# Optimization experiments

Hardware: AMD Instinct MI355X
Metric: run time of the kernel (lower is better)

Reference implementation:

```python
import jax, jax.numpy as jnp
import numpy as np

B, C, FULLBIN, T = 4, 2, 1025, 1024
BINS = 1024            # n_fft // 2
BANDS = 4
D = BINS // BANDS      # 256
FF = 2048
FF2, FF4 = FF // 2, FF // 4
CROP = 1024
EPS = 1e-5


def layernorm(x, g, b):
    m = jnp.mean(x, axis=-1, keepdims=True)
    v = jnp.mean(jnp.square(x - m), axis=-1, keepdims=True)
    return (x - m) * jax.lax.rsqrt(v + EPS) * g + b


def dconv(x, w, pad):
    # depthwise Conv1d: x (B, Cc, L), w (Cc, 1, K)
    return jax.lax.conv_general_dilated(
        x, w, window_strides=(1,), padding=[(pad, pad)],
        feature_group_count=x.shape[1],
        dimension_numbers=('NCH', 'OIH', 'NCH'))


def pconv(x, w):
    # pointwise Conv1d: x (B, Ci, L), w (Co, Ci, 1)
    return jnp.einsum('bcl,oc->bol', x, w[:, :, 0])


def reference(src, in_w, ln1_g, ln1_b, glu_w, ln2_g, ln2_b,
              c1L_dw, c1L_pw, c1R_dw, c1R_pw, ln3_g, ln3_b,
              c1M_dw, c1M_pw, ln4_g, ln4_b,
              q_w, q_b, qc_w, qc_b, k_w, k_b, v_w, v_b, o_w, o_b, er,
              ln5_g, ln5_b, c2_w, c3_w, out_w):
    s = src[:, :, :BINS]                                 # (B,C,F,T)
    x = jnp.einsum('bcft,c->btf', s, in_w[0])            # in_project + squeeze -> (B,T,BINS)

    # GLU block
    h = layernorm(x, ln1_g, ln1_b)
    g = h @ glu_w.T                                       # (B,T,2*BINS)
    x = x + g[..., :BINS] * jax.nn.sigmoid(g[..., BINS:])

    # conv feed-forward (note: conv1L applied without transpose, as in original)
    h = layernorm(x, ln2_g, ln2_b)
    hL = jax.nn.relu(pconv(dconv(h, c1L_dw, 5), c1L_pw))                          # (B,FF2,BINS)
    hR = jax.nn.relu(pconv(dconv(jnp.swapaxes(h, 1, 2), c1R_dw, 3), c1R_pw))      # (B,FF4,T)
    hR = jnp.swapaxes(hR, 1, 2)                                                   # (B,T,FF4)
    hR = jnp.pad(hR, ((0, 0), (0, 0), (0, BINS - FF4)))
    h = layernorm(hL + hR, ln3_g, ln3_b)                                          # (B,FF2,BINS)
    h = pconv(dconv(jnp.swapaxes(h, 1, 2), c1M_dw, 3), c1M_pw)                    # (B,BINS,FF2)
    x = x + jnp.swapaxes(h, 1, 2)

    # multiband frame attention (q_conv reused for q,k,v as in original)
    h = layernorm(x, ln4_g, ln4_b)

    def qkv(W, bvec):
        y = h @ W.T + bvec
        y = dconv(jnp.swapaxes(y, 1, 2), qc_w, 3) + qc_b[None, :, None]
        return jnp.swapaxes(y, 1, 2).reshape(B, T, BANDS, D)

    q = qkv(q_w, q_b).transpose(0, 2, 1, 3)              # (B,BANDS,T,D)
    k = qkv(k_w, k_b).transpose(0, 2, 3, 1)              # (B,BANDS,D,T)
    v = qkv(v_w, v_b).transpose(0, 2, 1, 3)              # (B,BANDS,T,D)

    p = jnp.pad(q @ er, ((0, 0), (0, 0), (0, 0), (1, 0)))  # (B,BANDS,T,CROP+1)
    p = jnp.swapaxes(p, 2, 3)[:, :, 1:, :]                 # (B,BANDS,CROP,T)
    qk = (q @ k + p) / jnp.sqrt(jnp.float32(BINS))
    a = jax.nn.softmax(qk, axis=-1)
    o = (a @ v).transpose(0, 2, 1, 3).reshape(B, T, BINS) @ o_w.T + o_b
    x = x + o

    # squared-ReLU MLP
    h = layernorm(x, ln5_g, ln5_b)
    h = jnp.square(jax.nn.relu(h @ c2_w.T)) @ c3_w.T
    x = x + h

    # stack back as extra channel, output head, ReLU1, replicate-pad freq row
    t = jnp.swapaxes(x, 1, 2)[:, None]                   # (B,1,BINS,T)
    s2 = jnp.concatenate([s, t], axis=1)                 # (B,C+1,BINS,T)
    y = jnp.einsum('bcft,oc->boft', s2, out_w)           # (B,2,BINS,T)
    y = jnp.clip(y, 0.0, 6.0) / 6.0
    return jnp.concatenate([y, y[:, :, -1:, :]], axis=2)  # (B,2,FULLBIN,T)


def setup_inputs() -> dict:
    key = jax.random.key(0)
    ks = jax.random.split(key, 20)
    n = lambda i, shape, s=0.02: jax.random.normal(ks[i], shape, jnp.float32) * s
    return {
        'src': jax.random.normal(ks[0], (B, C, FULLBIN, T), jnp.float32),
        'in_w': n(1, (1, C)),
        'ln1_g': jnp.ones((BINS,), jnp.float32), 'ln1_b': jnp.zeros((BINS,), jnp.float32),
        'glu_w': n(2, (2 * BINS, BINS)),
        'ln2_g': jnp.ones((BINS,), jnp.float32), 'ln2_b': jnp.zeros((BINS,), jnp.float32),
        'c1L_dw': n(3, (BINS, 1, 11), 0.1), 'c1L_pw': n(4, (FF2, BINS, 1)),
        'c1R_dw': n(5, (BINS, 1, 7), 0.1), 'c1R_pw': n(6, (FF4, BINS, 1)),
        'ln3_g': jnp.ones((FF2,), jnp.float32), 'ln3_b': jnp.zeros((FF2,), jnp.float32),
        'c1M_dw': n(7, (FF2, 1, 7), 0.1), 'c1M_pw': n(8, (BINS, FF2, 1)),
        'ln4_g': jnp.ones((BINS,), jnp.float32), 'ln4_b': jnp.zeros((BINS,), jnp.float32),
        'q_w': n(9, (BINS, BINS)), 'q_b': jnp.zeros((BINS,), jnp.float32),
        'qc_w': n(10, (BINS, 1, 7), 0.1), 'qc_b': jnp.zeros((BINS,), jnp.float32),
        'k_w': n(11, (BINS, BINS)), 'k_b': jnp.zeros((BINS,), jnp.float32),
        'v_w': n(12, (BINS, BINS)), 'v_b': jnp.zeros((BINS,), jnp.float32),
        'o_w': n(13, (BINS, BINS)), 'o_b': jnp.zeros((BINS,), jnp.float32),
        'er': jax.random.normal(ks[14], (D, CROP), jnp.float32),
        'ln5_g': jnp.ones((BINS,), jnp.float32), 'ln5_b': jnp.zeros((BINS,), jnp.float32),
        'c2_w': n(15, (FF, BINS)), 'c3_w': n(16, (BINS, FF)),
        'out_w': n(17, (2, C + 1)),
    }
```

## Files before the change

### kernel.cpp

```cpp
#include <hip/hip_runtime.h>
#include <math.h>


typedef unsigned short u16;
typedef __attribute__((ext_vector_type(4))) float floatx4;
typedef __attribute__((ext_vector_type(8))) short short8;

#define NB 4
static const long long M1 = 1024LL * 1024LL;

__device__ __forceinline__ float bf2f(u16 h) {
    union { unsigned int u; float f; } v;
    v.u = ((unsigned int)h) << 16;
    return v.f;
}
__device__ __forceinline__ u16 f2bf(float x) {
    union { float f; unsigned int u; } v;
    v.f = x;
    unsigned int r = (v.u + 0x7FFFu + ((v.u >> 16) & 1u)) >> 16;
    return (u16)r;
}

__device__ __forceinline__ void async_cp16(const u16* g, u16* lds) {
    __builtin_amdgcn_global_load_lds(
        (const __attribute__((address_space(1))) unsigned int*)g,
        (__attribute__((address_space(3))) unsigned int*)lds, 16, 0, 0);
}

__device__ __forceinline__ float block_sum(float v) {
    __shared__ float sd[4];
    #pragma unroll
    for (int off = 32; off; off >>= 1) v += __shfl_down(v, off, 64);
    int lane = threadIdx.x & 63, wid = threadIdx.x >> 6;
    __syncthreads();
    if (lane == 0) sd[wid] = v;
    __syncthreads();
    return sd[0] + sd[1] + sd[2] + sd[3];
}

template<int BM, int BN, int ACT, int OUT>
__global__ __launch_bounds__(256)
void gemm_bf(const u16* __restrict__ A, const u16* __restrict__ B,
             void* __restrict__ Cv, int K, int lda, int ldb, int ldc,
             long long sAz, long long sBz, long long sCz,
             const float* __restrict__ bias, float scale)
{
    constexpr int MI = BM / 32;
    constexpr int NJ = BN / 32;

    A += (long long)blockIdx.z * sAz;
    B += (long long)blockIdx.z * sBz;
    const long long zc = (long long)blockIdx.z * sCz;

    __shared__ u16 As[BM * 64];
    __shared__ u16 Bs[BN * 64];

    const int id = blockIdx.x + gridDim.x * blockIdx.y;
    const int bx = (id >> 3) % gridDim.x;
    const int by = (id & 7) + 8 * ((id >> 3) / gridDim.x);
    const int m0 = by * BM;
    const int n0 = bx * BN;

    const int lane = threadIdx.x & 63;
    const int w    = threadIdx.x >> 6;
    const int wm   = (w >> 1) * (BM / 2);
    const int wn   = (w & 1) * (BN / 2);
    const int srow = lane >> 2;
    const int scol = (lane & 3) * 8;

    floatx4 acc[MI][NJ];
    #pragma unroll
    for (int i = 0; i < MI; i++)
        #pragma unroll
        for (int j = 0; j < NJ; j++)
            acc[i][j] = floatx4{0.f, 0.f, 0.f, 0.f};

    for (int k0 = 0; k0 < K; k0 += 64) {
        #pragma unroll
        for (int r = 0; r < BM / 32; r++) {
            const int inst = w * (BM / 32) + r;
            const int rg = inst >> 1, kb = inst & 1;
            async_cp16(A + (long long)(m0 + rg * 16 + srow) * lda + k0 + kb * 32 + scol,
                       &As[(rg * 2 + kb) * 512]);
        }
        #pragma unroll
        for (int r = 0; r < BN / 32; r++) {
            const int inst = w * (BN / 32) + r;
            const int rg = inst >> 1, kb = inst & 1;
            async_cp16(B + (long long)(n0 + rg * 16 + srow) * ldb + k0 + kb * 32 + scol,
                       &Bs[(rg * 2 + kb) * 512]);
        }
        __syncthreads();

        #pragma unroll
        for (int s = 0; s < 2; s++) {
            short8 a[MI], b[NJ];
            const int fr = lane & 15;
            const int q  = lane >> 4;
            const int go = (fr * 4 + q) * 8;
            #pragma unroll
            for (int i = 0; i < MI; i++)
                a[i] = *(const short8*)&As[(((wm >> 4) + i) * 2 + s) * 512 + go];
            #pragma unroll
            for (int j = 0; j < NJ; j++)
                b[j] = *(const short8*)&Bs[(((wn >> 4) + j) * 2 + s) * 512 + go];
            #pragma unroll
            for (int i = 0; i < MI; i++)
                #pragma unroll
                for (int j = 0; j < NJ; j++)
                    acc[i][j] = __builtin_amdgcn_mfma_f32_16x16x32_bf16(
                        a[i], b[j], acc[i][j], 0, 0, 0);
        }
        __syncthreads();
    }

    float* Cf = (float*)Cv;
    u16*  Cb  = (u16*)Cv;
    const int cn    = n0 + wn + (lane & 15);
    const int rbase = m0 + wm + (lane >> 4) * 4;
    float bj[NJ];
    #pragma unroll
    for (int j = 0; j < NJ; j++) bj[j] = bias ? bias[cn + j * 16] : 0.f;

    #pragma unroll
    for (int i = 0; i < MI; i++) {
        #pragma unroll
        for (int r = 0; r < 4; r++) {
            const int m = rbase + i * 16 + r;
            #pragma unroll
            for (int j = 0; j < NJ; j++) {
                const int n = cn + j * 16;
                float v = (acc[i][j][r] + bj[j]) * scale;
                if (ACT == 1) v = fmaxf(v, 0.f);
                else if (ACT == 2) { v = fmaxf(v, 0.f); v = v * v; }
                const long long ci = zc + (long long)m * ldc + n;
                if (OUT == 0)      Cf[ci] = v;
                else if (OUT == 1) Cf[ci] += v;
                else if (OUT == 2) Cb[ci] = f2bf(v);
                else               Cb[ci] = f2bf(bf2f(Cb[ci]) + v);
            }
        }
    }
}

__global__ __launch_bounds__(256)
void glugemm_k(const u16* __restrict__ A, const u16* __restrict__ B1,
               const u16* __restrict__ B2, u16* __restrict__ X)
{
    constexpr int BM = 128, BN = 64, MI = 4, NJ = 2;
    __shared__ u16 As[BM * 64];
    __shared__ u16 B1s[BN * 64];
    __shared__ u16 B2s[BN * 64];

    const int id = blockIdx.x + gridDim.x * blockIdx.y;
    const int bx = (id >> 3) % gridDim.x;
    const int by = (id & 7) + 8 * ((id >> 3) / gridDim.x);
    const int m0 = by * BM;
    const int n0 = bx * BN;

    const int lane = threadIdx.x & 63;
    const int w    = threadIdx.x >> 6;
    const int wm   = (w >> 1) * 64;
    const int wn   = (w & 1) * 32;
    const int srow = lane >> 2;
    const int scol = (lane & 3) * 8;

    floatx4 acc1[MI][NJ], acc2[MI][NJ];
    #pragma unroll
    for (int i = 0; i < MI; i++)
        #pragma unroll
        for (int j = 0; j < NJ; j++) {
            acc1[i][j] = floatx4{0.f, 0.f, 0.f, 0.f};
            acc2[i][j] = floatx4{0.f, 0.f, 0.f, 0.f};
        }

    for (int k0 = 0; k0 < 1024; k0 += 64) {
        #pragma unroll
        for (int r = 0; r < 4; r++) {
            const int inst = w * 4 + r;
            const int rg = inst >> 1, kb = inst & 1;
            async_cp16(A + (long long)(m0 + rg * 16 + srow) * 1024 + k0 + kb * 32 + scol,
                       &As[(rg * 2 + kb) * 512]);
        }
        #pragma unroll
        for (int r = 0; r < 2; r++) {
            const int inst = w * 2 + r;
            const int rg = inst >> 1, kb = inst & 1;
            async_cp16(B1 + (long long)(n0 + rg * 16 + srow) * 1024 + k0 + kb * 32 + scol,
                       &B1s[(rg * 2 + kb) * 512]);
            async_cp16(B2 + (long long)(n0 + rg * 16 + srow) * 1024 + k0 + kb * 32 + scol,
                       &B2s[(rg * 2 + kb) * 512]);
        }
        __syncthreads();

        #pragma unroll
        for (int s = 0; s < 2; s++) {
            short8 a[MI], b1[NJ], b2[NJ];
            const int fr = lane & 15;
            const int q  = lane >> 4;
            const int go = (fr * 4 + q) * 8;
            #pragma unroll
            for (int i = 0; i < MI; i++)
                a[i] = *(const short8*)&As[(((wm >> 4) + i) * 2 + s) * 512 + go];
            #pragma unroll
            for (int j = 0; j < NJ; j++) {
                b1[j] = *(const short8*)&B1s[(((wn >> 4) + j) * 2 + s) * 512 + go];
                b2[j] = *(const short8*)&B2s[(((wn >> 4) + j) * 2 + s) * 512 + go];
            }
            #pragma unroll
            for (int i = 0; i < MI; i++)
                #pragma unroll
                for (int j = 0; j < NJ; j++) {
                    acc1[i][j] = __builtin_amdgcn_mfma_f32_16x16x32_bf16(
                        a[i], b1[j], acc1[i][j], 0, 0, 0);
                    acc2[i][j] = __builtin_amdgcn_mfma_f32_16x16x32_bf16(
                        a[i], b2[j], acc2[i][j], 0, 0, 0);
                }
        }
        __syncthreads();
    }

    const int cn    = n0 + wn + (lane & 15);
    const int rbase = m0 + wm + (lane >> 4) * 4;
    #pragma unroll
    for (int i = 0; i < MI; i++)
        #pragma unroll
        for (int r = 0; r < 4; r++) {
            const int m = rbase + i * 16 + r;
            #pragma unroll
            for (int j = 0; j < NJ; j++) {
                const int n = cn + j * 16;
                float g = acc1[i][j][r] / (1.f + expf(-acc2[i][j][r]));
                u16* xp = &X[(long long)m * 1024 + n];
                *xp = f2bf(bf2f(*xp) + g);
            }
        }
}

__global__ __launch_bounds__(256)
void sgemm_exp_k(const u16* __restrict__ Qpk, const u16* __restrict__ Kpk,
                 const u16* __restrict__ ErT,
                 u16* __restrict__ S, float* __restrict__ rowsum, float scale)
{
    constexpr int MI = 4, NJ = 4;
    const int i0 = blockIdx.x;
    const int x  = i0 & 7;
    const int j0 = i0 >> 3;
    const int z  = x + 8 * (j0 & 1);
    const int t  = j0 >> 1;
    const int bx = t & 7, by = t >> 3;

    const u16* Aq = Qpk + (long long)z * 262144;
    const u16* Bk = Kpk + (long long)z * 262144;
    S += (long long)z * M1;
    rowsum += z << 10;

    __shared__ u16 As[128 * 64];
    __shared__ u16 Bs[128 * 64];

    const int m0 = by * 128;
    const int n0 = bx * 128;

    const int lane = threadIdx.x & 63;
    const int w    = threadIdx.x >> 6;
    const int wm   = (w >> 1) * 64;
    const int wn   = (w & 1) * 64;
    const int srow = lane >> 2;
    const int scol = (lane & 3) * 8;

    floatx4 acc[MI][NJ];
    #pragma unroll
    for (int i = 0; i < MI; i++)
        #pragma unroll
        for (int j = 0; j < NJ; j++)
            acc[i][j] = floatx4{0.f, 0.f, 0.f, 0.f};

    for (int k0 = 0; k0 < 512; k0 += 64) {
        #pragma unroll
        for (int r = 0; r < 4; r++) {
            const int inst = w * 4 + r;
            const int rg = inst >> 1, kb = inst & 1;
            const int cb = k0 + kb * 32;
            const int ra = m0 + rg * 16 + srow;
            const u16* sa = (cb < 256)
                ? Aq  + (long long)ra * 256 + cb + scol
                : ErT + (long long)ra * 256 + (cb - 256) + scol;
            async_cp16(sa, &As[(rg * 2 + kb) * 512]);
            const int rb = n0 + rg * 16 + srow;
            const u16* sb = (cb < 256)
                ? Bk + (long long)rb * 256 + cb + scol
                : Aq + (long long)rb * 256 + (cb - 256) + scol;
            async_cp16(sb, &Bs[(rg * 2 + kb) * 512]);
        }
        __syncthreads();
        #pragma unroll
        for (int s = 0; s < 2; s++) {
            short8 a[MI], b[NJ];
            const int fr = lane & 15;
            const int q  = lane >> 4;
            const int go = (fr * 4 + q) * 8;
            #pragma unroll
            for (int i = 0; i < MI; i++)
                a[i] = *(const short8*)&As[(((wm >> 4) + i) * 2 + s) * 512 + go];
            #pragma unroll
            for (int j = 0; j < NJ; j++)
                b[j] = *(const short8*)&Bs[(((wn >> 4) + j) * 2 + s) * 512 + go];
            #pragma unroll
            for (int i = 0; i < MI; i++)
                #pragma unroll
                for (int j = 0; j < NJ; j++)
                    acc[i][j] = __builtin_amdgcn_mfma_f32_16x16x32_bf16(
                        a[i], b[j], acc[i][j], 0, 0, 0);
        }
        __syncthreads();
    }

    const int cn    = n0 + wn + (lane & 15);
    const int rbase = m0 + wm + (lane >> 4) * 4;
    #pragma unroll
    for (int i = 0; i < MI; i++)
        #pragma unroll
        for (int r = 0; r < 4; r++) {
            const int m = rbase + i * 16 + r;
            float part = 0.f;
            #pragma unroll
            for (int j = 0; j < NJ; j++) {
                const int n = cn + j * 16;
                float e = expf(acc[i][j][r] * scale);
                S[(long long)m * 1024 + n] = f2bf(e);
                part += e;
            }
            #pragma unroll
            for (int off = 8; off; off >>= 1) part += __shfl_xor(part, off, 64);
            if ((lane & 15) == 0) atomicAdd(&rowsum[m], part);
        }
}

__global__ __launch_bounds__(256)
void aogemm_k(const u16* __restrict__ Sb, const u16* __restrict__ Vt,
              const float* __restrict__ rowsum, u16* __restrict__ AO)
{
    constexpr int MI = 4, NJ = 2;
    const int i0 = blockIdx.x;
    const int x  = i0 & 7;
    const int j0 = i0 >> 3;
    const int z  = x + 8 * (j0 & 1);
    const int t  = j0 >> 1;
    const int bx = t & 3, by = t >> 2;

    Sb += (long long)z * M1;
    Vt += (long long)z * 262144;
    rowsum += z << 10;
    const long long zc = (long long)(z >> 2) * M1 + (z & 3) * 256;

    __shared__ u16 As[128 * 64];
    __shared__ u16 Bs[64 * 64];

    const int m0 = by * 128;
    const int n0 = bx * 64;

    const int lane = threadIdx.x & 63;
    const int w    = threadIdx.x >> 6;
    const int wm   = (w >> 1) * 64;
    const int wn   = (w & 1) * 32;
    const int srow = lane >> 2;
    const int scol = (lane & 3) * 8;

    floatx4 acc[MI][NJ];
    #pragma unroll
    for (int i = 0; i < MI; i++)
        #pragma unroll
        for (int j = 0; j < NJ; j++)
            acc[i][j] = floatx4{0.f, 0.f, 0.f, 0.f};

    for (int k0 = 0; k0 < 1024; k0 += 64) {
        #pragma unroll
        for (int r = 0; r < 4; r++) {
            const int inst = w * 4 + r;
            const int rg = inst >> 1, kb = inst & 1;
            async_cp16(Sb + (long long)(m0 + rg * 16 + srow) * 1024 + k0 + kb * 32 + scol,
                       &As[(rg * 2 + kb) * 512]);
        }
        #pragma unroll
        for (int r = 0; r < 2; r++) {
            const int inst = w * 2 + r;
            const int rg = inst >> 1, kb = inst & 1;
            async_cp16(Vt + (long long)(n0 + rg * 16 + srow) * 1024 + k0 + kb * 32 + scol,
                       &Bs[(rg * 2 + kb) * 512]);
        }
        __syncthreads();
        #pragma unroll
        for (int s = 0; s < 2; s++) {
            short8 a[MI], b[NJ];
            const int fr = lane & 15;
            const int q  = lane >> 4;
            const int go = (fr * 4 + q) * 8;
            #pragma unroll
            for (int i = 0; i < MI; i++)
                a[i] = *(const short8*)&As[(((wm >> 4) + i) * 2 + s) * 512 + go];
            #pragma unroll
            for (int j = 0; j < NJ; j++)
                b[j] = *(const short8*)&Bs[(((wn >> 4) + j) * 2 + s) * 512 + go];
            #pragma unroll
            for (int i = 0; i < MI; i++)
                #pragma unroll
                for (int j = 0; j < NJ; j++)
                    acc[i][j] = __builtin_amdgcn_mfma_f32_16x16x32_bf16(
                        a[i], b[j], acc[i][j], 0, 0, 0);
        }
        __syncthreads();
    }

    const int cn    = n0 + wn + (lane & 15);
    const int rbase = m0 + wm + (lane >> 4) * 4;
    #pragma unroll
    for (int i = 0; i < MI; i++)
        #pragma unroll
        for (int r = 0; r < 4; r++) {
            const int m = rbase + i * 16 + r;
            const float inv = 1.f / rowsum[m];
            #pragma unroll
            for (int j = 0; j < NJ; j++) {
                const int n = cn + j * 16;
                AO[zc + (long long)m * 1024 + n] = f2bf(acc[i][j][r] * inv);
            }
        }
}

__global__ __launch_bounds__(256)
void ln_bf_k(const u16* __restrict__ in, u16* __restrict__ out,
             const float* __restrict__ g, const float* __restrict__ b)
{
    long long row = blockIdx.x;
    int tid = threadIdx.x;
    ushort4 u = ((const ushort4*)(in + (row << 10)))[tid];
    float x0 = bf2f(u.x), x1 = bf2f(u.y), x2 = bf2f(u.z), x3 = bf2f(u.w);
    float s = x0 + x1 + x2 + x3;
    s = block_sum(s);
    float mean = s * (1.f / 1024.f);
    float dx = x0 - mean, dy = x1 - mean, dz = x2 - mean, dw = x3 - mean;
    float s2 = dx * dx + dy * dy + dz * dz + dw * dw;
    s2 = block_sum(s2);
    float inv = rsqrtf(s2 * (1.f / 1024.f) + 1e-5f);
    float4 gg = ((const float4*)g)[tid];
    float4 bb = ((const float4*)b)[tid];
    ushort4 o;
    o.x = f2bf(dx * inv * gg.x + bb.x);
    o.y = f2bf(dy * inv * gg.y + bb.y);
    o.z = f2bf(dz * inv * gg.z + bb.z);
    o.w = f2bf(dw * inv * gg.w + bb.w);
    ((ushort4*)(out + (row << 10)))[tid] = o;
}

struct CastArgs {
    const float* s[10];
    const float* er; const float* qb; const float* kb; const float* vb;
    u16* ert; float* qkvb;
};
__global__ __launch_bounds__(256)
void castin_k(CastArgs a, u16* __restrict__ dst,
              const float* __restrict__ src, const float* __restrict__ inw,
              u16* __restrict__ X)
{
    const int bid = blockIdx.x;
    if (bid < 24576) {
        const int sz[10] = {2097152, 1048576, 524288, 1048576, 1048576,
                            1048576, 1048576, 1048576, 2097152, 2097152};
        int seg = bid >> 11;
        int tid = (bid & 2047) * 256 + threadIdx.x;
        if (seg < 10) {
            int n = sz[seg];
            int base = 0;
            for (int i = 0; i < seg; i++) base += sz[i];
            int i4 = tid * 4;
            if (i4 >= n) return;
            float4 v = *(const float4*)(a.s[seg] + i4);
            ushort4 o;
            o.x = f2bf(v.x); o.y = f2bf(v.y); o.z = f2bf(v.z); o.w = f2bf(v.w);
            *(ushort4*)(dst + base + i4) = o;
        } else if (seg == 10) {
            if (tid < 262144) {
                int j = tid >> 8, d = tid & 255;
                a.ert[tid] = f2bf(a.er[d * 1024 + j]);
            }
        } else {
            if (tid < 1024) a.qkvb[tid] = a.qb[tid];
            else if (tid < 2048) a.qkvb[tid] = a.kb[tid - 1024];
            else if (tid < 3072) a.qkvb[tid] = a.vb[tid - 2048];
        }
    } else {
        __shared__ float tile[32][33];
        int ib = bid - 24576;
        int f0 = (ib & 31) * 32, t0 = ((ib >> 5) & 31) * 32, b = ib >> 10;
        int tx = threadIdx.x & 31, ty = threadIdx.x >> 5;
        float w0 = inw[0], w1 = inw[1];
        for (int r = ty; r < 32; r += 8) {
            int f = f0 + r, t = t0 + tx;
            float s0 = src[(((long long)b * 2 + 0) * 1025 + f) * 1024 + t];
            float s1 = src[(((long long)b * 2 + 1) * 1025 + f) * 1024 + t];
            tile[r][tx] = w0 * s0 + w1 * s1;
        }
        __syncthreads();
        for (int r = ty; r < 32; r += 8)
            X[((long long)b * 1024 + t0 + r) * 1024 + f0 + tx] = f2bf(tile[tx][r]);
    }
}

__global__ __launch_bounds__(256)
void dconvFT_k(const u16* __restrict__ in, u16* __restrict__ outT,
               const float* __restrict__ wT, u16* __restrict__ outF,
               const float* __restrict__ wF)
{
    const int bid = blockIdx.x;
    if (bid < 16384) {
        int idx = bid * 256 + threadIdx.x;
        int f = idx & 1023;
        int bt = idx >> 10;
        int t = bt & 1023;
        int b = bt >> 10;
        const float* wr = wT + f * 7;
        float acc = 0.f;
        #pragma unroll
        for (int k = 0; k < 7; k++) {
            int tt = t + k - 3;
            if (tt >= 0 && tt < 1024)
                acc += bf2f(in[(((long long)b << 10) + tt) * 1024 + f]) * wr[k];
        }
        outT[idx] = f2bf(acc);
    } else {
        __shared__ float itile[32][44];
        __shared__ float otile[32][33];
        int ib = bid - 16384;
        int f0 = (ib & 31) * 32, t0 = ((ib >> 5) & 31) * 32, b = ib >> 10;
        int tx = threadIdx.x & 31, ty = threadIdx.x >> 5;
        for (int r = ty; r < 32; r += 8)
            for (int c = tx; c < 42; c += 32) {
                int f = f0 - 5 + c;
                itile[r][c] = (f >= 0 && f < 1024)
                    ? bf2f(in[((long long)(b * 1024 + t0 + r)) * 1024 + f]) : 0.f;
            }
        __syncthreads();
        for (int r = ty; r < 32; r += 8) {
            const float* wr = wF + (t0 + r) * 11;
            float acc = 0.f;
            #pragma unroll
            for (int k = 0; k < 11; k++) acc += itile[r][tx + k] * wr[k];
            otile[tx][r] = acc;
        }
        __syncthreads();
        for (int r = ty; r < 32; r += 8)
            outF[((long long)(b * 1024 + f0 + r)) * 1024 + t0 + tx] = f2bf(otile[r][tx]);
    }
}

__global__ __launch_bounds__(256)
void dconvT_bf_k(const u16* __restrict__ in, u16* __restrict__ out,
                 const float* __restrict__ w)
{
    int idx = blockIdx.x * 256 + threadIdx.x;
    int f = idx & 1023;
    int bt = idx >> 10;
    int t = bt & 1023;
    int b = bt >> 10;
    const float* wr = w + f * 7;
    float acc = 0.f;
    #pragma unroll
    for (int k = 0; k < 7; k++) {
        int tt = t + k - 3;
        if (tt >= 0 && tt < 1024)
            acc += bf2f(in[(((long long)b << 10) + tt) * 1024 + f]) * wr[k];
    }
    out[idx] = f2bf(acc);
}

__global__ __launch_bounds__(256)
void qkvpack_k(const u16* __restrict__ T3, const float* __restrict__ w,
               const float* __restrict__ bias,
               u16* __restrict__ Qpk, u16* __restrict__ Kpk,
               u16* __restrict__ Vt, float* __restrict__ rowsum)
{
    const int bid = blockIdx.x;
    if (bid < 16384) {
        int idx = bid * 256 + threadIdx.x;
        int f = idx & 1023;
        int t = (idx >> 10) & 1023;
        int b = idx >> 20;
        int band = f >> 8, d = f & 255, z = (b << 2) | band;
        const float* wr = w + f * 7;
        float bq = bias[f];
        float aq = bq, ak = bq;
        #pragma unroll
        for (int k = 0; k < 7; k++) {
            int tt = t + k - 3;
            if (tt >= 0 && tt < 1024) {
                const u16* row = T3 + ((long long)(b << 10) + tt) * 3072 + f;
                float wk = wr[k];
                aq += bf2f(row[0]) * wk;
                ak += bf2f(row[1024]) * wk;
            }
        }
        long long base = (long long)z * 262144 + t * 256 + d;
        Qpk[base] = f2bf(aq);
        Kpk[base] = f2bf(ak);
    } else if (bid < 20480) {
        __shared__ float itile[38][32];
        __shared__ float otile[32][33];
        int vb = bid - 16384;
        int f0 = (vb & 31) * 32, t0 = ((vb >> 5) & 31) * 32, b = vb >> 10;
        int tx = threadIdx.x & 31, ty = threadIdx.x >> 5;
        for (int i = threadIdx.x; i < 38 * 32; i += 256) {
            int r = i >> 5, c = i & 31;
            int t = t0 - 3 + r;
            itile[r][c] = (t >= 0 && t < 1024)
                ? bf2f(T3[((long long)(b * 1024 + t)) * 3072 + 2048 + f0 + c]) : 0.f;
        }
        __syncthreads();
        for (int r = ty; r < 32; r += 8) {
            const float* wr = w + (f0 + tx) * 7;
            float acc = bias[f0 + tx];
            #pragma unroll
            for (int k = 0; k < 7; k++) acc += itile[r + k][tx] * wr[k];
            otile[tx][r] = acc;
        }
        __syncthreads();
        for (int r = ty; r < 32; r += 8)
            Vt[((long long)(b * 1024 + f0 + r)) * 1024 + t0 + tx] = f2bf(otile[r][tx]);
    } else {
        int i = (bid - 20480) * 256 + threadIdx.x;
        rowsum[i] = 0.f;
    }
}

__global__ __launch_bounds__(256)
void out_k(const float* __restrict__ src, const u16* __restrict__ X,
           const float* __restrict__ ow, float* __restrict__ out)
{
    __shared__ float tile[32][33];
    int b = blockIdx.z;
    int f0 = blockIdx.y * 32, t0 = blockIdx.x * 32;
    for (int r = threadIdx.y; r < 32; r += 8)
        tile[r][threadIdx.x] = bf2f(X[((long long)b * 1024 + t0 + r) * 1024 + f0 + threadIdx.x]);
    __syncthreads();
    float w00 = ow[0], w01 = ow[1], w02 = ow[2];
    float w10 = ow[3], w11 = ow[4], w12 = ow[5];
    for (int r = threadIdx.y; r < 32; r += 8) {
        int f = f0 + r, t = t0 + threadIdx.x;
        float s0 = src[(((long long)b * 2 + 0) * 1025 + f) * 1024 + t];
        float s1 = src[(((long long)b * 2 + 1) * 1025 + f) * 1024 + t];
        float xv = tile[threadIdx.x][r];
        float v0 = fminf(fmaxf(w00 * s0 + w01 * s1 + w02 * xv, 0.f), 6.f) * (1.f / 6.f);
        float v1 = fminf(fmaxf(w10 * s0 + w11 * s1 + w12 * xv, 0.f), 6.f) * (1.f / 6.f);
        out[(((long long)b * 2 + 0) * 1025 + f) * 1024 + t] = v0;
        out[(((long long)b * 2 + 1) * 1025 + f) * 1024 + t] = v1;
        if (f == 1023) {
            out[(((long long)b * 2 + 0) * 1025 + 1024) * 1024 + t] = v0;
            out[(((long long)b * 2 + 1) * 1025 + 1024) * 1024 + t] = v1;
        }
    }
}

extern "C" void kernel_launch(void* const* d_in, const int* in_sizes, int n_in,
                              void* d_out, int out_size, void* d_ws, size_t ws_size,
                              hipStream_t stream)
{
    const float* src    = (const float*)d_in[0];
    const float* in_w   = (const float*)d_in[1];
    const float* ln1_g  = (const float*)d_in[2];
    const float* ln1_b  = (const float*)d_in[3];
    const float* glu_w  = (const float*)d_in[4];
    const float* ln2_g  = (const float*)d_in[5];
    const float* ln2_b  = (const float*)d_in[6];
    const float* c1L_dw = (const float*)d_in[7];
    const float* c1L_pw = (const float*)d_in[8];
    const float* c1R_dw = (const float*)d_in[9];
    const float* c1R_pw = (const float*)d_in[10];
    const float* ln3_g  = (const float*)d_in[11];
    const float* ln3_b  = (const float*)d_in[12];
    const float* c1M_dw = (const float*)d_in[13];
    const float* c1M_pw = (const float*)d_in[14];
    const float* ln4_g  = (const float*)d_in[15];
    const float* ln4_b  = (const float*)d_in[16];
    const float* q_w    = (const float*)d_in[17];
    const float* q_b    = (const float*)d_in[18];
    const float* qc_w   = (const float*)d_in[19];
    const float* qc_b   = (const float*)d_in[20];
    const float* k_w    = (const float*)d_in[21];
    const float* k_b    = (const float*)d_in[22];
    const float* v_w    = (const float*)d_in[23];
    const float* v_b    = (const float*)d_in[24];
    const float* o_w    = (const float*)d_in[25];
    const float* o_b    = (const float*)d_in[26];
    const float* er     = (const float*)d_in[27];
    const float* ln5_g  = (const float*)d_in[28];
    const float* ln5_b  = (const float*)d_in[29];
    const float* c2_w   = (const float*)d_in[30];
    const float* c3_w   = (const float*)d_in[31];
    const float* out_w  = (const float*)d_in[32];
    float* out = (float*)d_out;

    const size_t MB = 1ull << 20;
    if (ws_size < 162 * MB) return;
    char* wsb = (char*)d_ws;
    u16* X       = (u16*)(wsb + 0);
    u16* SB      = (u16*)(wsb + 8 * MB);
    float* rowsum= (float*)(wsb + 16 * MB);
    u16* Qpk     = (u16*)(wsb + 32 * MB);
    u16* Kpk     = (u16*)(wsb + 40 * MB);
    u16* Hbf     = (u16*)(wsb + 64 * MB);
    u16* T1bf    = (u16*)(wsb + 72 * MB);
    u16* T3      = (u16*)(wsb + 72 * MB);
    u16* AO      = (u16*)(wsb + 80 * MB);
    u16* T2bf    = (u16*)(wsb + 96 * MB);
    u16* Vt      = (u16*)(wsb + 96 * MB);
    u16* Sbf     = (u16*)(wsb + 104 * MB);
    u16* Gbf     = (u16*)(wsb + 104 * MB);
    u16* W0      = (u16*)(wsb + 136 * MB);

    u16* glu_wb  = W0;
    u16* c1L_pwb = W0 + 2097152;
    u16* c1R_pwb = W0 + 3145728;
    u16* c1M_pwb = W0 + 3670016;
    u16* qkv_wb  = W0 + 4718592;
    u16* o_wb    = W0 + 7864320;
    u16* c2_wb   = W0 + 8912896;
    u16* c3_wb   = W0 + 11010048;
    u16* ertb    = W0 + 13107200;
    float* qkvb  = (float*)(W0 + 13369344);

    const dim3 blk256(256);
    const dim3 tgrid(32, 32, NB);
    const dim3 tblk(32, 8);
    const int EW = 16384;

    CastArgs ca;
    ca.s[0] = glu_w;  ca.s[1] = c1L_pw; ca.s[2] = c1R_pw; ca.s[3] = c1M_pw;
    ca.s[4] = q_w;    ca.s[5] = k_w;    ca.s[6] = v_w;    ca.s[7] = o_w;
    ca.s[8] = c2_w;   ca.s[9] = c3_w;
    ca.er = er; ca.qb = q_b; ca.kb = k_b; ca.vb = v_b;
    ca.ert = ertb; ca.qkvb = qkvb;
    castin_k<<<28672, blk256, 0, stream>>>(ca, W0, src, in_w, X);

    ln_bf_k<<<4096, blk256, 0, stream>>>(X, Hbf, ln1_g, ln1_b);
    glugemm_k<<<dim3(16, 32, 1), blk256, 0, stream>>>(
        Hbf, glu_wb, glu_wb + 1048576, X);
    ln_bf_k<<<4096, blk256, 0, stream>>>(X, Hbf, ln2_g, ln2_b);
    dconvFT_k<<<20480, blk256, 0, stream>>>(Hbf, T1bf, c1R_dw, T2bf, c1L_dw);
    gemm_bf<128, 64, 1, 2><<<dim3(16, 8, NB), blk256, 0, stream>>>(
        c1L_pwb, T2bf, SB, 1024, 1024, 1024, 1024, 0, M1, M1, nullptr, 1.f);
    gemm_bf<128, 64, 1, 3><<<dim3(8, 32, 1), blk256, 0, stream>>>(
        T1bf, c1R_pwb, SB, 1024, 1024, 1024, 1024, 0, 0, 0, nullptr, 1.f);
    ln_bf_k<<<4096, blk256, 0, stream>>>(SB, Hbf, ln3_g, ln3_b);
    dconvT_bf_k<<<EW, blk256, 0, stream>>>(Hbf, T1bf, c1M_dw);
    gemm_bf<128, 64, 0, 3><<<dim3(16, 32, 1), blk256, 0, stream>>>(
        T1bf, c1M_pwb, X, 1024, 1024, 1024, 1024, 0, 0, 0, nullptr, 1.f);
    ln_bf_k<<<4096, blk256, 0, stream>>>(X, Hbf, ln4_g, ln4_b);
    gemm_bf<128, 128, 0, 2><<<dim3(24, 32, 1), blk256, 0, stream>>>(
        Hbf, qkv_wb, T3, 1024, 1024, 1024, 3072, 0, 0, 0, qkvb, 1.f);
    qkvpack_k<<<20544, blk256, 0, stream>>>(T3, qc_w, qc_b, Qpk, Kpk, Vt, rowsum);
    sgemm_exp_k<<<1024, blk256, 0, stream>>>(Qpk, Kpk, ertb, Sbf, rowsum, 0.03125f);
    aogemm_k<<<512, blk256, 0, stream>>>(Sbf, Vt, rowsum, AO);
    gemm_bf<128, 64, 0, 3><<<dim3(16, 32, 1), blk256, 0, stream>>>(
        AO, o_wb, X, 1024, 1024, 1024, 1024, 0, 0, 0, o_b, 1.f);
    ln_bf_k<<<4096, blk256, 0, stream>>>(X, Hbf, ln5_g, ln5_b);
    gemm_bf<128, 128, 2, 2><<<dim3(16, 32, 1), blk256, 0, stream>>>(
        Hbf, c2_wb, Gbf, 1024, 1024, 1024, 2048, 0, 0, 0, nullptr, 1.f);
    gemm_bf<128, 64, 0, 3><<<dim3(16, 32, 1), blk256, 0, stream>>>(
        Gbf, c3_wb, X, 2048, 2048, 2048, 1024, 0, 0, 0, nullptr, 1.f);
    out_k<<<tgrid, tblk, 0, stream>>>(src, X, out_w, out);
}
```

Before: 570.5 us.

## Enlarge GEMM tiles to 128x128, split sgemm K-loop, use fast exp

Several output-projection and pointwise GEMMs move from 128x64 to 128x128 tiles, and aogemm_k moves to 128x128 tiles with half the blocks, so each loaded tile feeds more MFMA work. The sgemm_exp_k K loop is split into two separate loops, one for Q·K and one for Er·Q, which removes the per-iteration pointer select. expf is replaced with __expf in the GLU sigmoid and the softmax exp. The larger tiles cut the block count to as few as 256 on a chip with many CUs, which can lower occupancy and parallelism, and __expf gives slightly lower precision.

Measured after the change: 589.5 us. 1.03x slower.

```diff
diff --git a/kernel.cpp b/kernel.cpp
--- a/kernel.cpp
+++ b/kernel.cpp
@@ -230,12 +230,35 @@
             #pragma unroll
             for (int j = 0; j < NJ; j++) {
                 const int n = cn + j * 16;
-                float g = acc1[i][j][r] / (1.f + expf(-acc2[i][j][r]));
+                float g = acc1[i][j][r] / (1.f + __expf(-acc2[i][j][r]));
                 u16* xp = &X[(long long)m * 1024 + n];
                 *xp = f2bf(bf2f(*xp) + g);
             }
         }
 }
+
+#define SGEMM_MMA_STEP                                                        \
+    __syncthreads();                                                          \
+    _Pragma("unroll")                                                         \
+    for (int s = 0; s < 2; s++) {                                             \
+        short8 a[MI], b[NJ];                                                  \
+        const int fr = lane & 15;                                             \
+        const int q  = lane >> 4;                                             \
+        const int go = (fr * 4 + q) * 8;                                      \
+        _Pragma("unroll")                                                     \
+        for (int i = 0; i < MI; i++)                                          \
+            a[i] = *(const short8*)&As[(((wm >> 4) + i) * 2 + s) * 512 + go]; \
+        _Pragma("unroll")                                                     \
+        for (int j = 0; j < NJ; j++)                                          \
+            b[j] = *(const short8*)&Bs[(((wn >> 4) + j) * 2 + s) * 512 + go]; \
+        _Pragma("unroll")                                                     \
+        for (int i = 0; i < MI; i++)                                          \
+            _Pragma("unroll")                                                 \
+            for (int j = 0; j < NJ; j++)                                      \
+                acc[i][j] = __builtin_amdgcn_mfma_f32_16x16x32_bf16(          \
+                    a[i], b[j], acc[i][j], 0, 0, 0);                          \
+    }                                                                         \
+    __syncthreads();
 
 __global__ __launch_bounds__(256)
 void sgemm_exp_k(const u16* __restrict__ Qpk, const u16* __restrict__ Kpk,
@@ -275,44 +298,31 @@
         for (int j = 0; j < NJ; j++)
             acc[i][j] = floatx4{0.f, 0.f, 0.f, 0.f};
 
-    for (int k0 = 0; k0 < 512; k0 += 64) {
+    for (int k0 = 0; k0 < 256; k0 += 64) {
         #pragma unroll
         for (int r = 0; r < 4; r++) {
             const int inst = w * 4 + r;
             const int rg = inst >> 1, kb = inst & 1;
             const int cb = k0 + kb * 32;
-            const int ra = m0 + rg * 16 + srow;
-            const u16* sa = (cb < 256)
-                ? Aq  + (long long)ra * 256 + cb + scol
-                : ErT + (long long)ra * 256 + (cb - 256) + scol;
-            async_cp16(sa, &As[(rg * 2 + kb) * 512]);
-            const int rb = n0 + rg * 16 + srow;
-            const u16* sb = (cb < 256)
-                ? Bk + (long long)rb * 256 + cb + scol
-                : Aq + (long long)rb * 256 + (cb - 256) + scol;
-            async_cp16(sb, &Bs[(rg * 2 + kb) * 512]);
-        }
-        __syncthreads();
-        #pragma unroll
-        for (int s = 0; s < 2; s++) {
-            short8 a[MI], b[NJ];
-            const int fr = lane & 15;
-            const int q  = lane >> 4;
-            const int go = (fr * 4 + q) * 8;
-            #pragma unroll
-            for (int i = 0; i < MI; i++)
-                a[i] = *(const short8*)&As[(((wm >> 4) + i) * 2 + s) * 512 + go];
-            #pragma unroll
-            for (int j = 0; j < NJ; j++)
-                b[j] = *(const short8*)&Bs[(((wn >> 4) + j) * 2 + s) * 512 + go];
-            #pragma unroll
-            for (int i = 0; i < MI; i++)
-                #pragma unroll
-                for (int j = 0; j < NJ; j++)
-                    acc[i][j] = __builtin_amdgcn_mfma_f32_16x16x32_bf16(
-                        a[i], b[j], acc[i][j], 0, 0, 0);
-        }
-        __syncthreads();
+            async_cp16(Aq + (long long)(m0 + rg * 16 + srow) * 256 + cb + scol,
+                       &As[(rg * 2 + kb) * 512]);
+            async_cp16(Bk + (long long)(n0 + rg * 16 + srow) * 256 + cb + scol,
+                       &Bs[(rg * 2 + kb) * 512]);
+        }
+        SGEMM_MMA_STEP
+    }
+    for (int k0 = 0; k0 < 256; k0 += 64) {
+        #pragma unroll
+        for (int r = 0; r < 4; r++) {
+            const int inst = w * 4 + r;
+            const int rg = inst >> 1, kb = inst & 1;
+            const int cb = k0 + kb * 32;
+            async_cp16(ErT + (long long)(m0 + rg * 16 + srow) * 256 + cb + scol,
+                       &As[(rg * 2 + kb) * 512]);
+            async_cp16(Aq + (long long)(n0 + rg * 16 + srow) * 256 + cb + scol,
+                       &Bs[(rg * 2 + kb) * 512]);
+        }
+        SGEMM_MMA_STEP
     }
 
     const int cn    = n0 + wn + (lane & 15);
@@ -326,7 +336,7 @@
             #pragma unroll
             for (int j = 0; j < NJ; j++) {
                 const int n = cn + j * 16;
-                float e = expf(acc[i][j][r] * scale);
+                float e = __expf(acc[i][j][r] * scale);
                 S[(long long)m * 1024 + n] = f2bf(e);
                 part += e;
             }
@@ -340,13 +350,13 @@
 void aogemm_k(const u16* __restrict__ Sb, const u16* __restrict__ Vt,
               const float* __restrict__ rowsum, u16* __restrict__ AO)
 {
-    constexpr int MI = 4, NJ = 2;
+    constexpr int MI = 4, NJ = 4;
     const int i0 = blockIdx.x;
     const int x  = i0 & 7;
     const int j0 = i0 >> 3;
     const int z  = x + 8 * (j0 & 1);
     const int t  = j0 >> 1;
-    const int bx = t & 3, by = t >> 2;
+    const int bx = t & 1, by = t >> 1;
 
     Sb += (long long)z * M1;
     Vt += (long long)z * 262144;
@@ -354,15 +364,15 @@
     const long long zc = (long long)(z >> 2) * M1 + (z & 3) * 256;
 
     __shared__ u16 As[128 * 64];
-    __shared__ u16 Bs[64 * 64];
+    __shared__ u16 Bs[128 * 64];
 
     const int m0 = by * 128;
-    const int n0 = bx * 64;
+    const int n0 = bx * 128;
 
     const int lane = threadIdx.x & 63;
     const int w    = threadIdx.x >> 6;
     const int wm   = (w >> 1) * 64;
-    const int wn   = (w & 1) * 32;
+    const int wn   = (w & 1) * 64;
     const int srow = lane >> 2;
     const int scol = (lane & 3) * 8;
 
@@ -380,35 +390,10 @@
             const int rg = inst >> 1, kb = inst & 1;
             async_cp16(Sb + (long long)(m0 + rg * 16 + srow) * 1024 + k0 + kb * 32 + scol,
                        &As[(rg * 2 + kb) * 512]);
-        }
-        #pragma unroll
-        for (int r = 0; r < 2; r++) {
-            const int inst = w * 2 + r;
-            const int rg = inst >> 1, kb = inst & 1;
             async_cp16(Vt + (long long)(n0 + rg * 16 + srow) * 1024 + k0 + kb * 32 + scol,
                        &Bs[(rg * 2 + kb) * 512]);
         }
-        __syncthreads();
-        #pragma unroll
-        for (int s = 0; s < 2; s++) {
-            short8 a[MI], b[NJ];
-            const int fr = lane & 15;
-            const int q  = lane >> 4;
-            const int go = (fr * 4 + q) * 8;
-            #pragma unroll
-            for (int i = 0; i < MI; i++)
-                a[i] = *(const short8*)&As[(((wm >> 4) + i) * 2 + s) * 512 + go];
-            #pragma unroll
-            for (int j = 0; j < NJ; j++)
-                b[j] = *(const short8*)&Bs[(((wn >> 4) + j) * 2 + s) * 512 + go];
-            #pragma unroll
-            for (int i = 0; i < MI; i++)
-                #pragma unroll
-                for (int j = 0; j < NJ; j++)
-                    acc[i][j] = __builtin_amdgcn_mfma_f32_16x16x32_bf16(
-                        a[i], b[j], acc[i][j], 0, 0, 0);
-        }
-        __syncthreads();
+        SGEMM_MMA_STEP
     }
 
     const int cn    = n0 + wn + (lane & 15);
@@ -745,26 +730,26 @@
         Hbf, glu_wb, glu_wb + 1048576, X);
     ln_bf_k<<<4096, blk256, 0, stream>>>(X, Hbf, ln2_g, ln2_b);
     dconvFT_k<<<20480, blk256, 0, stream>>>(Hbf, T1bf, c1R_dw, T2bf, c1L_dw);
-    gemm_bf<128, 64, 1, 2><<<dim3(16, 8, NB), blk256, 0, stream>>>(
+    gemm_bf<128, 128, 1, 2><<<dim3(8, 8, NB), blk256, 0, stream>>>(
         c1L_pwb, T2bf, SB, 1024, 1024, 1024, 1024, 0, M1, M1, nullptr, 1.f);
     gemm_bf<128, 64, 1, 3><<<dim3(8, 32, 1), blk256, 0, stream>>>(
         T1bf, c1R_pwb, SB, 1024, 1024, 1024, 1024, 0, 0, 0, nullptr, 1.f);
     ln_bf_k<<<4096, blk256, 0, stream>>>(SB, Hbf, ln3_g, ln3_b);
     dconvT_bf_k<<<EW, blk256, 0, stream>>>(Hbf, T1bf, c1M_dw);
-    gemm_bf<128, 64, 0, 3><<<dim3(16, 32, 1), blk256, 0, stream>>>(
+    gemm_bf<128, 128, 0, 3><<<dim3(8, 32, 1), blk256, 0, stream>>>(
         T1bf, c1M_pwb, X, 1024, 1024, 1024, 1024, 0, 0, 0, nullptr, 1.f);
     ln_bf_k<<<4096, blk256, 0, stream>>>(X, Hbf, ln4_g, ln4_b);
     gemm_bf<128, 128, 0, 2><<<dim3(24, 32, 1), blk256, 0, stream>>>(
         Hbf, qkv_wb, T3, 1024, 1024, 1024, 3072, 0, 0, 0, qkvb, 1.f);
     qkvpack_k<<<20544, blk256, 0, stream>>>(T3, qc_w, qc_b, Qpk, Kpk, Vt, rowsum);
     sgemm_exp_k<<<1024, blk256, 0, stream>>>(Qpk, Kpk, ertb, Sbf, rowsum, 0.03125f);
-    aogemm_k<<<512, blk256, 0, stream>>>(Sbf, Vt, rowsum, AO);
-    gemm_bf<128, 64, 0, 3><<<dim3(16, 32, 1), blk256, 0, stream>>>(
+    aogemm_k<<<256, blk256, 0, stream>>>(Sbf, Vt, rowsum, AO);
+    gemm_bf<128, 128, 0, 3><<<dim3(8, 32, 1), blk256, 0, stream>>>(
         AO, o_wb, X, 1024, 1024, 1024, 1024, 0, 0, 0, o_b, 1.f);
     ln_bf_k<<<4096, blk256, 0, stream>>>(X, Hbf, ln5_g, ln5_b);
     gemm_bf<128, 128, 2, 2><<<dim3(16, 32, 1), blk256, 0, stream>>>(
         Hbf, c2_wb, Gbf, 1024, 1024, 1024, 2048, 0, 0, 0, nullptr, 1.f);
-    gemm_bf<128, 64, 0, 3><<<dim3(16, 32, 1), blk256, 0, stream>>>(
+    gemm_bf<128, 128, 0, 3><<<dim3(8, 32, 1), blk256, 0, stream>>>(
         Gbf, c3_wb, X, 2048, 2048, 2048, 1024, 0, 0, 0, nullptr, 1.f);
     out_k<<<tgrid, tblk, 0, stream>>>(src, X, out_w, out);
 }
```
